# Kernel tuning notes

Hardware: AMD Instinct MI355X
Metric: run time of the kernel (lower is better)

Reference implementation:

```python
import jax, jax.numpy as jnp
import numpy as np

N = 20000      # interaction nodes
E = 160000     # edges
NU = 100000    # num_users
NI = 100000    # num_items
EMB = 64       # emb_size
L1, L2 = 256, 128  # GCN layer dims
H = 2          # GAT heads (and number of GAT layers)
EPS = 1e-5


def _seg(x, idx, n):
    return jax.ops.segment_sum(x, idx, num_segments=n)


def _gcn(x, W, b, src, dst, n):
    # GCNConv: add self-loops, sym-normalize, aggregate src->dst
    loops = jnp.arange(n)
    s = jnp.concatenate([src, loops])
    d = jnp.concatenate([dst, loops])
    deg = _seg(jnp.ones(s.shape[0], x.dtype), d, n)
    dinv = jnp.where(deg > 0, 1.0 / jnp.sqrt(deg), 0.0)
    xw = x @ W
    return _seg((dinv[s] * dinv[d])[:, None] * xw[s], d, n) + b


def _bn(x, g, b):
    # BatchNorm1d in training mode: biased batch statistics
    mu = x.mean(0)
    var = x.var(0)
    return (x - mu) / jnp.sqrt(var + EPS) * g + b


def _sage(x, Wl, bl, Wr, src, dst, n):
    # SAGEConv: mean neighbor aggregation (no self loops) + root transform
    cnt = _seg(jnp.ones(src.shape[0], x.dtype), dst, n)
    agg = _seg(x[src], dst, n) / jnp.maximum(cnt, 1.0)[:, None]
    return agg @ Wl + bl + x @ Wr


def _cheb(x, W0, W1c, b, src, dst, n):
    # ChebConv K=2, lambda_max=2: Tx0 = x, Tx1 = -D^{-1/2} A D^{-1/2} x
    deg = _seg(jnp.ones(src.shape[0], x.dtype), dst, n)
    dinv = jnp.where(deg > 0, 1.0 / jnp.sqrt(deg), 0.0)
    tx1 = -_seg((dinv[src] * dinv[dst])[:, None] * x[src], dst, n)
    return x @ W0 + tx1 @ W1c + b


def _gat(x, W, a_s, a_d, b, src, dst, n):
    # GATConv: add self-loops, per-edge attention softmax over dst, concat=False -> mean over heads
    loops = jnp.arange(n)
    s = jnp.concatenate([src, loops])
    d = jnp.concatenate([dst, loops])
    xp = (x @ W).reshape(n, H, L2)           # [n, H, C]
    al = (xp * a_s).sum(-1)                  # [n, H]
    ar = (xp * a_d).sum(-1)                  # [n, H]
    e = jax.nn.leaky_relu(al[s] + ar[d], 0.2)  # [E', H]
    m = jax.lax.stop_gradient(jax.ops.segment_max(e, d, num_segments=n))
    ex = jnp.exp(e - m[d])
    alpha = ex / _seg(ex, d, n)[d]
    out = _seg(alpha[:, :, None] * xp[s], d, n)  # [n, H, C]
    return out.mean(1) + b


def setup_inputs() -> dict:
    key = jax.random.key(0)
    ks = jax.random.split(key, 40)
    f = lambda k, shp: jax.random.normal(k, shp, dtype=jnp.float32) * 0.02
    inp = {
        'user_idx': jax.random.randint(ks[0], (N,), 0, NU, dtype=jnp.int32),
        'item_idx': jax.random.randint(ks[1], (N,), 0, NI, dtype=jnp.int32),
        'edge_index': jax.random.randint(ks[2], (2, E), 0, N, dtype=jnp.int32),
        'user_emb': f(ks[3], (NU, EMB)),
        'item_emb': f(ks[4], (NI, EMB)),
        'W1': f(ks[5], (2 * EMB, 1024)), 'b1': f(ks[6], (1024,)),
        'W2': f(ks[7], (1024, 512)), 'b2': f(ks[8], (512,)),
        'Wg1': f(ks[9], (512, L1)), 'bg1': f(ks[10], (L1,)),
        'gamma1': 1.0 + f(ks[11], (L1,)), 'beta1': f(ks[12], (L1,)),
        'Wg2': f(ks[13], (L1, L2)), 'bg2': f(ks[14], (L2,)),
        'gamma2': 1.0 + f(ks[15], (L2,)), 'beta2': f(ks[16], (L2,)),
        'Wsl': f(ks[17], (L2, L2)), 'bsl': f(ks[18], (L2,)),
        'Wsr': f(ks[19], (L2, L2)),
        'Wc0': f(ks[20], (L2, L2)), 'Wc1': f(ks[21], (L2, L2)), 'bc': f(ks[22], (L2,)),
        'Wgat1': f(ks[23], (L2, H * L2)), 'as1': f(ks[24], (H, L2)), 'ad1': f(ks[25], (H, L2)), 'bgat1': f(ks[26], (L2,)),
        'Wgat2': f(ks[27], (L2, H * L2)), 'as2': f(ks[28], (H, L2)), 'ad2': f(ks[29], (H, L2)), 'bgat2': f(ks[30], (L2,)),
        'Wp': f(ks[31], (L2, 1)), 'bp': f(ks[32], (1,)),
    }
    return inp


def reference(user_idx, item_idx, edge_index, user_emb, item_emb, W1, b1, W2, b2,
              Wg1, bg1, gamma1, beta1, Wg2, bg2, gamma2, beta2,
              Wsl, bsl, Wsr, Wc0, Wc1, bc,
              Wgat1, as1, ad1, bgat1, Wgat2, as2, ad2, bgat2, Wp, bp):
    src, dst = edge_index[0], edge_index[1]
    n = user_idx.shape[0]
    x = jnp.concatenate([user_emb[user_idx], item_emb[item_idx]], axis=1)
    # MLP (dropout is identity in eval mode)
    x = jax.nn.relu(x @ W1 + b1)
    x = jax.nn.relu(x @ W2 + b2)
    x = jax.nn.relu(_bn(_gcn(x, Wg1, bg1, src, dst, n), gamma1, beta1))
    x = jax.nn.relu(_bn(_gcn(x, Wg2, bg2, src, dst, n), gamma2, beta2))
    x = jax.nn.relu(_sage(x, Wsl, bsl, Wsr, src, dst, n))
    x = jax.nn.relu(_cheb(x, Wc0, Wc1, bc, src, dst, n))
    x = jax.nn.elu(_gat(x, Wgat1, as1, ad1, bgat1, src, dst, n))
    x = jax.nn.elu(_gat(x, Wgat2, as2, ad2, bgat2, src, dst, n))
    return (x @ Wp + bp)[:, 0]
```

## Files before the change

kernel.cpp:

```cpp
#include <hip/hip_runtime.h>
#include <hip/hip_bf16.h>

typedef __hip_bfloat16 bf16;
typedef short s8v __attribute__((ext_vector_type(8)));
typedef float f4v __attribute__((ext_vector_type(4)));

#define NN 20000
#define NE 160000
#define BN_EPS 1e-5f
#define NB 79

#define GF_BIAS 1
#define GF_RELU 2

static __device__ __forceinline__ float b2f(const bf16 x){ return __bfloat162float(x); }
static __device__ __forceinline__ float bits2f(unsigned int u){ return __uint_as_float(u << 16); }
static __device__ __forceinline__ unsigned short f2bits(float f){
  bf16 h = __float2bfloat16(f);
  unsigned short u; __builtin_memcpy(&u, &h, 2); return u;
}
static __device__ __forceinline__ float lrelu(float v){ return (v > 0.f) ? v : 0.2f * v; }

static inline int cdiv(int a, int b){ return (a + b - 1) / b; }


__global__ void k_chk_bf(const unsigned short* __restrict__ x, int n, int code,
                         int* __restrict__ diag){
  bool bad = false;
  for (int k = blockIdx.x * 256 + threadIdx.x; k < n; k += gridDim.x * 256)
    if ((x[k] & 0x7F80u) == 0x7F80u) bad = true;
  if (bad) atomicCAS(diag, 0, code);
}

__global__ void k_diag_out(const int* __restrict__ diag, float* __restrict__ out){
  int d = *diag;
  if (d == 0) return;
  int i = blockIdx.x * 256 + threadIdx.x;
  if (i < NN) out[i] = (float)(d * 100);
}


__global__ void k_ideg(const int* __restrict__ dst, int* __restrict__ ideg){
  int e = blockIdx.x * 256 + threadIdx.x;
  if (e < NE) atomicAdd(&ideg[dst[e]], 1);
}

__global__ __launch_bounds__(256) void k_scan1(const int* __restrict__ ideg,
                                               int* __restrict__ tmp,
                                               int* __restrict__ bsum){
  __shared__ int lds[256];
  int tid = threadIdx.x;
  int i = blockIdx.x * 256 + tid;
  int v = (i < NN) ? ideg[i] : 0;
  lds[tid] = v;
  __syncthreads();
  for (int off = 1; off < 256; off <<= 1){
    int t = (tid >= off) ? lds[tid - off] : 0;
    __syncthreads();
    lds[tid] += t;
    __syncthreads();
  }
  if (i < NN) tmp[i] = lds[tid];
  if (tid == 255) bsum[blockIdx.x] = lds[255];
}

__global__ __launch_bounds__(128) void k_scan2(const int* __restrict__ bsum,
                                               int* __restrict__ boff){
  __shared__ int lds[128];
  int tid = threadIdx.x;
  int v = (tid < NB) ? bsum[tid] : 0;
  lds[tid] = v;
  __syncthreads();
  for (int off = 1; off < 128; off <<= 1){
    int t = (tid >= off) ? lds[tid - off] : 0;
    __syncthreads();
    lds[tid] += t;
    __syncthreads();
  }
  if (tid < NB) boff[tid] = lds[tid] - v;
}

__global__ __launch_bounds__(256) void k_scan3(const int* __restrict__ ideg,
                                               const int* __restrict__ boff,
                                               int* __restrict__ rowptr,
                                               int* __restrict__ cursor,
                                               float* __restrict__ dg,
                                               float* __restrict__ dc,
                                               float* __restrict__ ic){
  int i = blockIdx.x * 256 + threadIdx.x;
  if (i == 0) rowptr[NN] = NE;
  if (i >= NN) return;
  int v = ideg[i];
  int excl = cursor[i] - v + boff[blockIdx.x];
  rowptr[i] = excl;
  cursor[i] = excl;
  float d = (float)v;
  dg[i] = rsqrtf(d + 1.0f);
  dc[i] = (d > 0.f) ? rsqrtf(d) : 0.f;
  ic[i] = 1.0f / fmaxf(d, 1.0f);
}

__global__ void k_fill(const int* __restrict__ src, const int* __restrict__ dst,
                       int* __restrict__ cursor, int* __restrict__ colsrc){
  int e = blockIdx.x * 256 + threadIdx.x;
  if (e >= NE) return;
  int pos = atomicAdd(&cursor[dst[e]], 1);
  colsrc[pos] = src[e];
}


struct WtPack {
  const float* W[10]; short* hi[10]; short* lo[10];
  int K[10]; int nshift[10]; int base[11];
};

__global__ __launch_bounds__(256) void k_wtall(WtPack p){
  int idx = blockIdx.x * 256 + threadIdx.x;
  if (idx >= p.base[10]) return;
  int seg = 0;
#pragma unroll
  for (int i = 1; i < 10; i++) seg += (idx >= p.base[i]) ? 1 : 0;
  int local = idx - p.base[seg];
  int K = p.K[seg], ns = p.nshift[seg];
  int n = local & ((1 << ns) - 1), k = local >> ns;
  float w = p.W[seg][local];
  unsigned short h = f2bits(w);
  unsigned short l = f2bits(w - bits2f(h));
  p.hi[seg][(size_t)n * K + k] = (short)h;
  p.lo[seg][(size_t)n * K + k] = (short)l;
}


__global__ void k_gather(const int* __restrict__ uidx, const int* __restrict__ iidx,
                         const float* __restrict__ ue, const float* __restrict__ ie,
                         bf16* __restrict__ x0){
  int idx = blockIdx.x * 256 + threadIdx.x;
  if (idx >= NN * 128) return;
  int i = idx >> 7, c = idx & 127;
  float v = (c < 64) ? ue[(size_t)uidx[i] * 64 + c] : ie[(size_t)iidx[i] * 64 + (c - 64)];
  x0[idx] = __float2bfloat16(v);
}


__global__ __launch_bounds__(256) void k_mm64(
    const bf16* A0, const short* B0h, const short* B0l, int K0,
    const bf16* A1, const short* B1h, const short* B1l, int K1,
    const float* __restrict__ bias, bf16* __restrict__ C,
    int M, int Ncol, int flags, int npass){
  __shared__ short As[64][72];
  __shared__ short Bhs[64][72];
  __shared__ short Bls[64][72];
  const int tid = threadIdx.x;
  const int bid = blockIdx.y * gridDim.x + blockIdx.x;
  const int total = gridDim.x * gridDim.y;
  const int L = (bid & 7) * (total >> 3) + (bid >> 3);
  const int row0 = (L / gridDim.x) * 64, col0 = (L % gridDim.x) * 64;
  if (row0 >= M) return;
  const int wid = tid >> 6, lane = tid & 63;
  const int wr = (wid >> 1) * 32, wc = (wid & 1) * 32;
  const int lr = lane & 15, lq = lane >> 4;
  const int sr = tid >> 2, sq = (tid & 3) * 16;

  f4v acc[2][2];
#pragma unroll
  for (int i = 0; i < 2; i++)
#pragma unroll
    for (int j = 0; j < 2; j++)
      acc[i][j] = f4v{0.f, 0.f, 0.f, 0.f};

  const bf16* Aarr[2] = {A0, A1};
  const short* Bharr[2] = {B0h, B1h};
  const short* Blarr[2] = {B0l, B1l};
  const int Karr[2] = {K0, K1};

  const bool arow_ok = (row0 + sr) < M;

  for (int p = 0; p < npass; p++){
    const short* A = (const short*)Aarr[p];
    const short* Bh = Bharr[p];
    const short* Bl = Blarr[p];
    const int K = Karr[p];
    const short* arow = A + (size_t)(row0 + sr) * K + sq;
    const short* bhrow = Bh + (size_t)(col0 + sr) * K + sq;
    const short* blrow = Bl + (size_t)(col0 + sr) * K + sq;

    uint4 ra0 = make_uint4(0,0,0,0), ra1 = make_uint4(0,0,0,0);
    if (arow_ok){ ra0 = *(const uint4*)(arow); ra1 = *(const uint4*)(arow + 8); }
    uint4 rb0 = *(const uint4*)(bhrow), rb1 = *(const uint4*)(bhrow + 8);
    uint4 rc0 = *(const uint4*)(blrow), rc1 = *(const uint4*)(blrow + 8);

    for (int k0 = 0; k0 < K; k0 += 64){
      *(uint4*)&As[sr][sq] = ra0;  *(uint4*)&As[sr][sq + 8] = ra1;
      *(uint4*)&Bhs[sr][sq] = rb0; *(uint4*)&Bhs[sr][sq + 8] = rb1;
      *(uint4*)&Bls[sr][sq] = rc0; *(uint4*)&Bls[sr][sq + 8] = rc1;
      __syncthreads();
      if (k0 + 64 < K){
        int off = k0 + 64;
        if (arow_ok){ ra0 = *(const uint4*)(arow + off); ra1 = *(const uint4*)(arow + off + 8); }
        rb0 = *(const uint4*)(bhrow + off); rb1 = *(const uint4*)(bhrow + off + 8);
        rc0 = *(const uint4*)(blrow + off); rc1 = *(const uint4*)(blrow + off + 8);
      }
#pragma unroll
      for (int t = 0; t < 2; t++){
        s8v a[2], bh2[2], bl2[2];
#pragma unroll
        for (int i = 0; i < 2; i++) a[i] = *(const s8v*)&As[wr + i * 16 + lr][t * 32 + lq * 8];
#pragma unroll
        for (int j = 0; j < 2; j++){
          bh2[j] = *(const s8v*)&Bhs[wc + j * 16 + lr][t * 32 + lq * 8];
          bl2[j] = *(const s8v*)&Bls[wc + j * 16 + lr][t * 32 + lq * 8];
        }
#pragma unroll
        for (int i = 0; i < 2; i++)
#pragma unroll
          for (int j = 0; j < 2; j++){
            acc[i][j] = __builtin_amdgcn_mfma_f32_16x16x32_bf16(a[i], bh2[j], acc[i][j], 0, 0, 0);
            acc[i][j] = __builtin_amdgcn_mfma_f32_16x16x32_bf16(a[i], bl2[j], acc[i][j], 0, 0, 0);
          }
      }
      __syncthreads();
    }
  }

#pragma unroll
  for (int i = 0; i < 2; i++){
#pragma unroll
    for (int rg = 0; rg < 4; rg++){
      int row = row0 + wr + i * 16 + lq * 4 + rg;
      if (row >= M) continue;
#pragma unroll
      for (int j = 0; j < 2; j++){
        int col = col0 + wc + j * 16 + lr;
        float v = acc[i][j][rg];
        if (flags & GF_BIAS) v += bias[col];
        if (flags & GF_RELU) v = fmaxf(v, 0.f);
        C[(size_t)row * Ncol + col] = __float2bfloat16(v);
      }
    }
  }
}


__global__ __launch_bounds__(256) void k_agg(
    const int* __restrict__ rowptr, const int* __restrict__ colsrc,
    const bf16* __restrict__ x, const float* __restrict__ wn,
    const float* __restrict__ icv, const float* __restrict__ bias,
    float* __restrict__ outf, bf16* __restrict__ outb,
    int qshift, int mode){
  int idx = blockIdx.x * 256 + threadIdx.x;
  int total = NN << qshift;
  if (idx >= total) return;
  int d = idx >> qshift, q = idx & ((1 << qshift) - 1);
  int F = 4 << qshift;
  int c = q * 4;
  int r0 = rowptr[d], r1 = rowptr[d + 1];
  float s0 = 0.f, s1 = 0.f, s2 = 0.f, s3 = 0.f;
  const short* xs = (const short*)x;
  for (int r = r0; r < r1; r += 4){
    int n = r1 - r;
    int i0 = colsrc[r];
    int i1 = (n > 1) ? colsrc[r + 1] : 0;
    int i2 = (n > 2) ? colsrc[r + 2] : 0;
    int i3 = (n > 3) ? colsrc[r + 3] : 0;
    float w0 = (mode == 1) ? 1.f : wn[i0];
    float w1 = (n > 1) ? ((mode == 1) ? 1.f : wn[i1]) : 0.f;
    float w2 = (n > 2) ? ((mode == 1) ? 1.f : wn[i2]) : 0.f;
    float w3 = (n > 3) ? ((mode == 1) ? 1.f : wn[i3]) : 0.f;
    uint2 v0 = *(const uint2*)(xs + (size_t)i0 * F + c);
    uint2 v1 = *(const uint2*)(xs + (size_t)i1 * F + c);
    uint2 v2 = *(const uint2*)(xs + (size_t)i2 * F + c);
    uint2 v3 = *(const uint2*)(xs + (size_t)i3 * F + c);
    s0 += w0 * bits2f(v0.x & 0xffffu) + w1 * bits2f(v1.x & 0xffffu)
        + w2 * bits2f(v2.x & 0xffffu) + w3 * bits2f(v3.x & 0xffffu);
    s1 += w0 * bits2f(v0.x >> 16) + w1 * bits2f(v1.x >> 16)
        + w2 * bits2f(v2.x >> 16) + w3 * bits2f(v3.x >> 16);
    s2 += w0 * bits2f(v0.y & 0xffffu) + w1 * bits2f(v1.y & 0xffffu)
        + w2 * bits2f(v2.y & 0xffffu) + w3 * bits2f(v3.y & 0xffffu);
    s3 += w0 * bits2f(v0.y >> 16) + w1 * bits2f(v1.y >> 16)
        + w2 * bits2f(v2.y >> 16) + w3 * bits2f(v3.y >> 16);
  }
  if (mode == 0){
    float w = wn[d], w2 = w * w;
    uint2 vd = *(const uint2*)(xs + (size_t)d * F + c);
    float4 o;
    o.x = w * s0 + w2 * bits2f(vd.x & 0xffffu) + bias[c + 0];
    o.y = w * s1 + w2 * bits2f(vd.x >> 16)     + bias[c + 1];
    o.z = w * s2 + w2 * bits2f(vd.y & 0xffffu) + bias[c + 2];
    o.w = w * s3 + w2 * bits2f(vd.y >> 16)     + bias[c + 3];
    *(float4*)(outf + (size_t)d * F + c) = o;
  } else {
    float m = (mode == 1) ? icv[d] : -wn[d];
    unsigned int lo = (unsigned int)f2bits(s0 * m) | ((unsigned int)f2bits(s1 * m) << 16);
    unsigned int hi = (unsigned int)f2bits(s2 * m) | ((unsigned int)f2bits(s3 * m) << 16);
    *(uint2*)((short*)outb + (size_t)d * F + c) = make_uint2(lo, hi);
  }
}


__global__ void k_bn_stats(const float* __restrict__ x, float* __restrict__ stats, int F){
  int c = threadIdx.x & (F - 1);
  int rsub = threadIdx.x / F;
  int rpi = 256 / F;
  int r0 = blockIdx.x * 128;
  int rend = min(NN, r0 + 128);
  float s1 = 0.f, s2 = 0.f;
  for (int r = r0 + rsub; r < rend; r += rpi){
    float v = x[(size_t)r * F + c];
    s1 += v; s2 += v * v;
  }
  atomicAdd(&stats[c], s1);
  atomicAdd(&stats[F + c], s2);
}

__global__ void k_bn_apply(const float* __restrict__ x, const float* __restrict__ stats,
                           const float* __restrict__ g, const float* __restrict__ b,
                           int fshift, int total, bf16* __restrict__ out){
  int idx = blockIdx.x * 256 + threadIdx.x;
  if (idx >= total) return;
  int F = 1 << fshift;
  int c = idx & (F - 1);
  float mu = stats[c] * (1.0f / NN);
  float var = fmaxf(stats[F + c] * (1.0f / NN) - mu * mu, 0.f);
  float v = (x[idx] - mu) * rsqrtf(var + BN_EPS) * g[c] + b[c];
  out[idx] = __float2bfloat16(fmaxf(v, 0.f));
}


__global__ __launch_bounds__(256) void k_gat_alar(const bf16* __restrict__ xp,
                                                  const float* __restrict__ as_,
                                                  const float* __restrict__ ad_,
                                                  float* __restrict__ al,
                                                  float* __restrict__ ar){
  int d = blockIdx.x * 4 + (threadIdx.x >> 6);
  int lane = threadIdx.x & 63;
  if (d >= NN) return;
  int c0 = lane * 2;
  unsigned int p0 = *(const unsigned int*)((const short*)xp + (size_t)d * 256 + c0);
  unsigned int p1 = *(const unsigned int*)((const short*)xp + (size_t)d * 256 + 128 + c0);
  float x00 = bits2f(p0 & 0xffffu), x01 = bits2f(p0 >> 16);
  float x10 = bits2f(p1 & 0xffffu), x11 = bits2f(p1 >> 16);
  float sa0 = x00 * as_[c0] + x01 * as_[c0 + 1];
  float sd0 = x00 * ad_[c0] + x01 * ad_[c0 + 1];
  float sa1 = x10 * as_[128 + c0] + x11 * as_[128 + c0 + 1];
  float sd1 = x10 * ad_[128 + c0] + x11 * ad_[128 + c0 + 1];
#pragma unroll
  for (int off = 32; off > 0; off >>= 1){
    sa0 += __shfl_xor(sa0, off); sd0 += __shfl_xor(sd0, off);
    sa1 += __shfl_xor(sa1, off); sd1 += __shfl_xor(sd1, off);
  }
  if (lane == 0){
    al[d * 2] = sa0;     ar[d * 2] = sd0;
    al[d * 2 + 1] = sa1; ar[d * 2 + 1] = sd1;
  }
}

__global__ __launch_bounds__(64) void k_gat(const int* __restrict__ rowptr,
                                            const int* __restrict__ colsrc,
                                            const bf16* __restrict__ xp,
                                            const float* __restrict__ al,
                                            const float* __restrict__ ar,
                                            const float* __restrict__ bias,
                                            bf16* __restrict__ outb,
                                            const float* __restrict__ wp,
                                            const float* __restrict__ bp,
                                            float* __restrict__ outf){
  __shared__ float w0s[64], w1s[64];
  __shared__ int ss[64];
  int d = blockIdx.x;
  int lane = threadIdx.x;
  int r0 = rowptr[d], r1 = rowptr[d + 1];
  float ard0 = ar[d * 2], ard1 = ar[d * 2 + 1];
  float e0 = lrelu(al[d * 2] + ard0);
  float e1 = lrelu(al[d * 2 + 1] + ard1);
  float mx0 = e0, mx1 = e1;
  for (int r = r0 + lane; r < r1; r += 64){
    int s = colsrc[r];
    mx0 = fmaxf(mx0, lrelu(al[s * 2] + ard0));
    mx1 = fmaxf(mx1, lrelu(al[s * 2 + 1] + ard1));
  }
#pragma unroll
  for (int off = 32; off > 0; off >>= 1){
    mx0 = fmaxf(mx0, __shfl_xor(mx0, off));
    mx1 = fmaxf(mx1, __shfl_xor(mx1, off));
  }
  float ps0 = (lane == 0) ? expf(e0 - mx0) : 0.f;
  float ps1 = (lane == 0) ? expf(e1 - mx1) : 0.f;
  for (int r = r0 + lane; r < r1; r += 64){
    int s = colsrc[r];
    ps0 += expf(lrelu(al[s * 2] + ard0) - mx0);
    ps1 += expf(lrelu(al[s * 2 + 1] + ard1) - mx1);
  }
#pragma unroll
  for (int off = 32; off > 0; off >>= 1){
    ps0 += __shfl_xor(ps0, off);
    ps1 += __shfl_xor(ps1, off);
  }
  int c0 = lane * 2;
  float a00, a01, a10, a11;
  {
    float w0 = expf(e0 - mx0), w1 = expf(e1 - mx1);
    unsigned int p0 = *(const unsigned int*)((const short*)xp + (size_t)d * 256 + c0);
    unsigned int p1 = *(const unsigned int*)((const short*)xp + (size_t)d * 256 + 128 + c0);
    a00 = w0 * bits2f(p0 & 0xffffu); a01 = w0 * bits2f(p0 >> 16);
    a10 = w1 * bits2f(p1 & 0xffffu); a11 = w1 * bits2f(p1 >> 16);
  }
  for (int t0 = r0; t0 < r1; t0 += 64){
    int nt = min(64, r1 - t0);
    __syncthreads();
    if (lane < nt){
      int s = colsrc[t0 + lane];
      ss[lane] = s;
      w0s[lane] = expf(lrelu(al[s * 2] + ard0) - mx0);
      w1s[lane] = expf(lrelu(al[s * 2 + 1] + ard1) - mx1);
    }
    __syncthreads();
    for (int r = 0; r < nt; r++){
      int s = ss[r];
      float w0 = w0s[r], w1 = w1s[r];
      unsigned int p0 = *(const unsigned int*)((const short*)xp + (size_t)s * 256 + c0);
      unsigned int p1 = *(const unsigned int*)((const short*)xp + (size_t)s * 256 + 128 + c0);
      a00 += w0 * bits2f(p0 & 0xffffu); a01 += w0 * bits2f(p0 >> 16);
      a10 += w1 * bits2f(p1 & 0xffffu); a11 += w1 * bits2f(p1 >> 16);
    }
  }
  float v0 = 0.5f * (a00 / ps0 + a10 / ps1) + bias[c0];
  float v1 = 0.5f * (a01 / ps0 + a11 / ps1) + bias[c0 + 1];
  v0 = (v0 > 0.f) ? v0 : expm1f(v0);
  v1 = (v1 > 0.f) ? v1 : expm1f(v1);
  if (wp == nullptr){
    unsigned int packed = (unsigned int)f2bits(v0) | ((unsigned int)f2bits(v1) << 16);
    *(unsigned int*)((short*)outb + (size_t)d * 128 + c0) = packed;
  } else {
    float pv = v0 * wp[c0] + v1 * wp[c0 + 1];
#pragma unroll
    for (int off = 32; off > 0; off >>= 1) pv += __shfl_down(pv, off);
    if (lane == 0) outf[d] = pv + bp[0];
  }
}


extern "C" void kernel_launch(void* const* d_in, const int* in_sizes, int n_in,
                              void* d_out, int out_size, void* d_ws, size_t ws_size,
                              hipStream_t stream){
  const int* uidx = (const int*)d_in[0];
  const int* iidx = (const int*)d_in[1];
  const int* eidx = (const int*)d_in[2];
  const int* src = eidx;
  const int* dst = eidx + NE;
  const float* ue  = (const float*)d_in[3];
  const float* ie  = (const float*)d_in[4];
  const float* W1  = (const float*)d_in[5];  const float* b1  = (const float*)d_in[6];
  const float* W2  = (const float*)d_in[7];  const float* b2  = (const float*)d_in[8];
  const float* Wg1 = (const float*)d_in[9];  const float* bg1 = (const float*)d_in[10];
  const float* gamma1 = (const float*)d_in[11]; const float* beta1 = (const float*)d_in[12];
  const float* Wg2 = (const float*)d_in[13]; const float* bg2 = (const float*)d_in[14];
  const float* gamma2 = (const float*)d_in[15]; const float* beta2 = (const float*)d_in[16];
  const float* Wsl = (const float*)d_in[17]; const float* bsl = (const float*)d_in[18];
  const float* Wsr = (const float*)d_in[19];
  const float* Wc0 = (const float*)d_in[20]; const float* Wc1 = (const float*)d_in[21];
  const float* bc  = (const float*)d_in[22];
  const float* Wgat1 = (const float*)d_in[23]; const float* as1 = (const float*)d_in[24];
  const float* ad1 = (const float*)d_in[25];   const float* bgat1 = (const float*)d_in[26];
  const float* Wgat2 = (const float*)d_in[27]; const float* as2 = (const float*)d_in[28];
  const float* ad2 = (const float*)d_in[29];   const float* bgat2 = (const float*)d_in[30];
  const float* Wp  = (const float*)d_in[31];   const float* bp  = (const float*)d_in[32];

  int* diag   = (int*)d_ws;
  int* ideg   = diag + 4;
  float* stats1 = (float*)(ideg + NN);
  float* stats2 = stats1 + 512;
  int* bsum   = (int*)(stats2 + 256);
  int* boff   = bsum + 128;
  int* rowptr = boff + 128;
  int* cursor = rowptr + NN + 4;
  int* colsrc = cursor + NN;
  float* dg = (float*)(colsrc + NE);
  float* dc = dg + NN;
  float* ic = dc + NN;
  float* al = ic + NN;
  float* ar = al + 2 * NN;
  short* w1h = (short*)(ar + 2 * NN);
  short* w1l = w1h + 131072;
  short* w2h = w1l + 131072;
  short* w2l = w2h + 524288;
  short* wg1h = w2l + 524288;
  short* wg1l = wg1h + 131072;
  short* wg2h = wg1l + 131072;
  short* wg2l = wg2h + 32768;
  short* wslh = wg2l + 32768;
  short* wsll = wslh + 16384;
  short* wsrh = wsll + 16384;
  short* wsrl = wsrh + 16384;
  short* wc0h = wsrl + 16384;
  short* wc0l = wc0h + 16384;
  short* wc1h = wc0l + 16384;
  short* wc1l = wc1h + 16384;
  short* wgat1h = wc1l + 16384;
  short* wgat1l = wgat1h + 32768;
  short* wgat2h = wgat1l + 32768;
  short* wgat2l = wgat2h + 32768;
  short* X0 = wgat2l + 32768;
  short* H1 = X0 + (size_t)NN * 128;
  short* H2 = H1 + (size_t)10000 * 1024;

  bf16* x0b  = (bf16*)X0;
  bf16* h1b  = (bf16*)H1;
  bf16* h2b  = (bf16*)H2;
  bf16* xw1b = (bf16*)H1;
  float* g1f = (float*)H2;
  bf16* g1b  = (bf16*)(H1 + (size_t)NN * 256);
  bf16* xw2b = (bf16*)X0;
  float* x3f = (float*)H1;
  bf16* x3b  = (bf16*)H2;
  bf16* aggb = (bf16*)X0;
  bf16* x4b  = (bf16*)(H2 + (size_t)NN * 128);
  bf16* tx1b = (bf16*)X0;
  bf16* x5b  = (bf16*)(H2 + (size_t)NN * 256);
  bf16* xpb  = (bf16*)H1;
  bf16* x6b  = (bf16*)X0;

  auto mm = [&](const bf16* A1, const short* B1h, const short* B1l, int K1,
                const bf16* A2, const short* B2h, const short* B2l, int K2,
                const float* bias, bf16* C, int M, int N, int flags){
    int nx = N / 64;
    int ny = cdiv(M, 64);
    while ((nx * ny) & 7) ny++;
    dim3 g(nx, ny);
    int np = A2 ? 2 : 1;
    k_mm64<<<g, 256, 0, stream>>>(A1, B1h, B1l, K1, A2, B2h, B2l, K2,
                                  bias, C, M, N, flags, np);
  };

  hipMemsetAsync(diag, 0, (size_t)(4 + NN + 768) * 4, stream);

  k_ideg<<<cdiv(NE, 256), 256, 0, stream>>>(dst, ideg);
  k_scan1<<<NB, 256, 0, stream>>>(ideg, cursor, bsum);
  k_scan2<<<1, 128, 0, stream>>>(bsum, boff);
  k_scan3<<<NB, 256, 0, stream>>>(ideg, boff, rowptr, cursor, dg, dc, ic);
  k_fill<<<cdiv(NE, 256), 256, 0, stream>>>(src, dst, cursor, colsrc);

  {
    WtPack p;
    const float* Ws[10] = {W1, W2, Wg1, Wg2, Wsl, Wsr, Wc0, Wc1, Wgat1, Wgat2};
    short* his[10] = {w1h, w2h, wg1h, wg2h, wslh, wsrh, wc0h, wc1h, wgat1h, wgat2h};
    short* los[10] = {w1l, w2l, wg1l, wg2l, wsll, wsrl, wc0l, wc1l, wgat1l, wgat2l};
    int Ks[10] = {128, 1024, 512, 256, 128, 128, 128, 128, 128, 128};
    int nss[10] = {10, 9, 8, 7, 7, 7, 7, 7, 8, 8};
    int off = 0;
    for (int i = 0; i < 10; i++){
      p.W[i] = Ws[i]; p.hi[i] = his[i]; p.lo[i] = los[i];
      p.K[i] = Ks[i]; p.nshift[i] = nss[i]; p.base[i] = off;
      off += Ks[i] << nss[i];
    }
    p.base[10] = off;
    k_wtall<<<cdiv(off, 256), 256, 0, stream>>>(p);
  }

  k_gather<<<cdiv(NN * 128, 256), 256, 0, stream>>>(uidx, iidx, ue, ie, x0b);

  for (int ofs = 0; ofs < NN; ofs += 10000){
    mm(x0b + (size_t)ofs * 128, w1h, w1l, 128, nullptr, nullptr, nullptr, 0,
       b1, h1b, 10000, 1024, GF_BIAS | GF_RELU);
    mm(h1b, w2h, w2l, 1024, nullptr, nullptr, nullptr, 0,
       b2, h2b + (size_t)ofs * 512, 10000, 512, GF_BIAS | GF_RELU);
  }

  mm(h2b, wg1h, wg1l, 512, nullptr, nullptr, nullptr, 0, nullptr, xw1b, NN, 256, 0);
  k_agg<<<cdiv(NN * 64, 256), 256, 0, stream>>>(rowptr, colsrc, xw1b, dg, nullptr, bg1, g1f, nullptr, 6, 0);
  k_bn_stats<<<cdiv(NN, 128), 256, 0, stream>>>(g1f, stats1, 256);
  k_bn_apply<<<cdiv(NN * 256, 256), 256, 0, stream>>>(g1f, stats1, gamma1, beta1, 8, NN * 256, g1b);

  mm(g1b, wg2h, wg2l, 256, nullptr, nullptr, nullptr, 0, nullptr, xw2b, NN, 128, 0);
  k_agg<<<cdiv(NN * 32, 256), 256, 0, stream>>>(rowptr, colsrc, xw2b, dg, nullptr, bg2, x3f, nullptr, 5, 0);
  k_bn_stats<<<cdiv(NN, 128), 256, 0, stream>>>(x3f, stats2, 128);
  k_bn_apply<<<cdiv(NN * 128, 256), 256, 0, stream>>>(x3f, stats2, gamma2, beta2, 7, NN * 128, x3b);

  k_agg<<<cdiv(NN * 32, 256), 256, 0, stream>>>(rowptr, colsrc, x3b, nullptr, ic, nullptr, nullptr, aggb, 5, 1);
  mm(aggb, wslh, wsll, 128, x3b, wsrh, wsrl, 128, bsl, x4b, NN, 128, GF_BIAS | GF_RELU);

  k_agg<<<cdiv(NN * 32, 256), 256, 0, stream>>>(rowptr, colsrc, x4b, dc, nullptr, nullptr, nullptr, tx1b, 5, 2);
  mm(x4b, wc0h, wc0l, 128, tx1b, wc1h, wc1l, 128, bc, x5b, NN, 128, GF_BIAS | GF_RELU);

  mm(x5b, wgat1h, wgat1l, 128, nullptr, nullptr, nullptr, 0, nullptr, xpb, NN, 256, 0);
  k_gat_alar<<<cdiv(NN, 4), 256, 0, stream>>>(xpb, as1, ad1, al, ar);
  k_gat<<<NN, 64, 0, stream>>>(rowptr, colsrc, xpb, al, ar, bgat1, x6b,
                               nullptr, nullptr, nullptr);
  k_chk_bf<<<256, 256, 0, stream>>>((const unsigned short*)x6b, NN * 128, 16, diag);

  mm(x6b, wgat2h, wgat2l, 128, nullptr, nullptr, nullptr, 0, nullptr, xpb, NN, 256, 0);
  k_gat_alar<<<cdiv(NN, 4), 256, 0, stream>>>(xpb, as2, ad2, al, ar);
  k_gat<<<NN, 64, 0, stream>>>(rowptr, colsrc, xpb, al, ar, bgat2, nullptr,
                               Wp, bp, (float*)d_out);
  k_diag_out<<<cdiv(NN, 256), 256, 0, stream>>>(diag, (float*)d_out);
}
```

Baseline: 613.1 us.

## Add 128x128-tile MFMA GEMM with direct global-to-LDS loads for wide matmuls

Adds a new GEMM kernel that gives each block a 128x128 output tile, with each wave computing 64x64 through 4x4 MFMA fragments. Operands are staged into LDS with the global_load_lds builtin instead of going through registers. The MLP, first GCN and GAT projection matmuls move to this kernel to get more reuse per LDS load and fewer blocks. The larger tile uses 48KB of LDS per block and more accumulator registers, which can lower occupancy. There is no double buffering, and the N=256 cases launch few column tiles.

```diff
diff --git a/kernel.cpp b/kernel.cpp
--- a/kernel.cpp
+++ b/kernel.cpp
@@ -22,6 +22,12 @@
 static __device__ __forceinline__ float lrelu(float v){ return (v > 0.f) ? v : 0.2f * v; }
 
 static inline int cdiv(int a, int b){ return (a + b - 1) / b; }
+
+static __device__ __forceinline__ void gload16(const short* g, short* l){
+  __builtin_amdgcn_global_load_lds(
+      (const __attribute__((address_space(1))) unsigned int*)g,
+      (__attribute__((address_space(3))) unsigned int*)l, 16, 0, 0);
+}
 
 
 __global__ void k_chk_bf(const unsigned short* __restrict__ x, int n, int code,
@@ -231,6 +237,93 @@
 #pragma unroll
       for (int j = 0; j < 2; j++){
         int col = col0 + wc + j * 16 + lr;
+        float v = acc[i][j][rg];
+        if (flags & GF_BIAS) v += bias[col];
+        if (flags & GF_RELU) v = fmaxf(v, 0.f);
+        C[(size_t)row * Ncol + col] = __float2bfloat16(v);
+      }
+    }
+  }
+}
+
+
+__global__ __launch_bounds__(256) void k_mm128(
+    const bf16* A0, const short* B0h, const short* B0l, int K,
+    const float* __restrict__ bias, bf16* __restrict__ C,
+    int M, int Ncol, int flags){
+  __shared__ short As[128 * 64];
+  __shared__ short Bhs[128 * 64];
+  __shared__ short Bls[128 * 64];
+  const int tid = threadIdx.x;
+  const int bid = blockIdx.y * gridDim.x + blockIdx.x;
+  const int total = gridDim.x * gridDim.y;
+  const int L = (bid & 7) * (total >> 3) + (bid >> 3);
+  const int row0 = (L / gridDim.x) * 128, col0 = (L % gridDim.x) * 128;
+  if (row0 >= M) return;
+  const int wid = tid >> 6, lane = tid & 63;
+  const int wr2 = (wid >> 1) * 64, wc2 = (wid & 1) * 64;
+  const int lr = lane & 15, lq = lane >> 4;
+
+  f4v acc[4][4];
+#pragma unroll
+  for (int i = 0; i < 4; i++)
+#pragma unroll
+    for (int j = 0; j < 4; j++)
+      acc[i][j] = f4v{0.f, 0.f, 0.f, 0.f};
+
+  const short* A = (const short*)A0;
+  const short* asrc[4]; const short* bhsrc[4]; const short* blsrc[4];
+  int sdst[4];
+#pragma unroll
+  for (int i = 0; i < 4; i++){
+    int ci = i * 256 + tid;
+    int r = ci >> 3, sg = ci & 7;
+    int ar = row0 + r; if (ar > M - 1) ar = M - 1;
+    asrc[i]  = A   + (size_t)ar * K + sg * 8;
+    bhsrc[i] = B0h + (size_t)(col0 + r) * K + sg * 8;
+    blsrc[i] = B0l + (size_t)(col0 + r) * K + sg * 8;
+    sdst[i] = ci * 8;
+  }
+
+  for (int k0 = 0; k0 < K; k0 += 64){
+    __syncthreads();
+#pragma unroll
+    for (int i = 0; i < 4; i++){
+      gload16(asrc[i]  + k0, As  + sdst[i]);
+      gload16(bhsrc[i] + k0, Bhs + sdst[i]);
+      gload16(blsrc[i] + k0, Bls + sdst[i]);
+    }
+    __syncthreads();
+#pragma unroll
+    for (int t = 0; t < 2; t++){
+      s8v a[4], bh2[4], bl2[4];
+#pragma unroll
+      for (int i = 0; i < 4; i++)
+        a[i] = *(const s8v*)&As[(wr2 + i * 16 + lr) * 64 + t * 32 + lq * 8];
+#pragma unroll
+      for (int j = 0; j < 4; j++){
+        bh2[j] = *(const s8v*)&Bhs[(wc2 + j * 16 + lr) * 64 + t * 32 + lq * 8];
+        bl2[j] = *(const s8v*)&Bls[(wc2 + j * 16 + lr) * 64 + t * 32 + lq * 8];
+      }
+#pragma unroll
+      for (int i = 0; i < 4; i++)
+#pragma unroll
+        for (int j = 0; j < 4; j++){
+          acc[i][j] = __builtin_amdgcn_mfma_f32_16x16x32_bf16(a[i], bh2[j], acc[i][j], 0, 0, 0);
+          acc[i][j] = __builtin_amdgcn_mfma_f32_16x16x32_bf16(a[i], bl2[j], acc[i][j], 0, 0, 0);
+        }
+    }
+  }
+
+#pragma unroll
+  for (int i = 0; i < 4; i++){
+#pragma unroll
+    for (int rg = 0; rg < 4; rg++){
+      int row = row0 + wr2 + i * 16 + lq * 4 + rg;
+      if (row >= M) continue;
+#pragma unroll
+      for (int j = 0; j < 4; j++){
+        int col = col0 + wc2 + j * 16 + lr;
         float v = acc[i][j][rg];
         if (flags & GF_BIAS) v += bias[col];
         if (flags & GF_RELU) v = fmaxf(v, 0.f);
@@ -531,6 +624,15 @@
                                   bias, C, M, N, flags, np);
   };
 
+  auto mm128 = [&](const bf16* A, const short* Bh, const short* Bl, int K,
+                   const float* bias, bf16* C, int M, int N, int flags){
+    int nx = N / 128;
+    int ny = cdiv(M, 128);
+    while ((nx * ny) & 7) ny++;
+    dim3 g(nx, ny);
+    k_mm128<<<g, 256, 0, stream>>>(A, Bh, Bl, K, bias, C, M, N, flags);
+  };
+
   hipMemsetAsync(diag, 0, (size_t)(4 + NN + 768) * 4, stream);
 
   k_ideg<<<cdiv(NE, 256), 256, 0, stream>>>(dst, ideg);
@@ -559,13 +661,13 @@
   k_gather<<<cdiv(NN * 128, 256), 256, 0, stream>>>(uidx, iidx, ue, ie, x0b);
 
   for (int ofs = 0; ofs < NN; ofs += 10000){
-    mm(x0b + (size_t)ofs * 128, w1h, w1l, 128, nullptr, nullptr, nullptr, 0,
-       b1, h1b, 10000, 1024, GF_BIAS | GF_RELU);
-    mm(h1b, w2h, w2l, 1024, nullptr, nullptr, nullptr, 0,
-       b2, h2b + (size_t)ofs * 512, 10000, 512, GF_BIAS | GF_RELU);
-  }
-
-  mm(h2b, wg1h, wg1l, 512, nullptr, nullptr, nullptr, 0, nullptr, xw1b, NN, 256, 0);
+    mm128(x0b + (size_t)ofs * 128, w1h, w1l, 128,
+          b1, h1b, 10000, 1024, GF_BIAS | GF_RELU);
+    mm128(h1b, w2h, w2l, 1024,
+          b2, h2b + (size_t)ofs * 512, 10000, 512, GF_BIAS | GF_RELU);
+  }
+
+  mm128(h2b, wg1h, wg1l, 512, nullptr, xw1b, NN, 256, 0);
   k_agg<<<cdiv(NN * 64, 256), 256, 0, stream>>>(rowptr, colsrc, xw1b, dg, nullptr, bg1, g1f, nullptr, 6, 0);
   k_bn_stats<<<cdiv(NN, 128), 256, 0, stream>>>(g1f, stats1, 256);
   k_bn_apply<<<cdiv(NN * 256, 256), 256, 0, stream>>>(g1f, stats1, gamma1, beta1, 8, NN * 256, g1b);
@@ -581,13 +683,13 @@
   k_agg<<<cdiv(NN * 32, 256), 256, 0, stream>>>(rowptr, colsrc, x4b, dc, nullptr, nullptr, nullptr, tx1b, 5, 2);
   mm(x4b, wc0h, wc0l, 128, tx1b, wc1h, wc1l, 128, bc, x5b, NN, 128, GF_BIAS | GF_RELU);
 
-  mm(x5b, wgat1h, wgat1l, 128, nullptr, nullptr, nullptr, 0, nullptr, xpb, NN, 256, 0);
+  mm128(x5b, wgat1h, wgat1l, 128, nullptr, xpb, NN, 256, 0);
   k_gat_alar<<<cdiv(NN, 4), 256, 0, stream>>>(xpb, as1, ad1, al, ar);
   k_gat<<<NN, 64, 0, stream>>>(rowptr, colsrc, xpb, al, ar, bgat1, x6b,
                                nullptr, nullptr, nullptr);
   k_chk_bf<<<256, 256, 0, stream>>>((const unsigned short*)x6b, NN * 128, 16, diag);
 
-  mm(x6b, wgat2h, wgat2l, 128, nullptr, nullptr, nullptr, 0, nullptr, xpb, NN, 256, 0);
+  mm128(x6b, wgat2h, wgat2l, 128, nullptr, xpb, NN, 256, 0);
   k_gat_alar<<<cdiv(NN, 4), 256, 0, stream>>>(xpb, as2, ad2, al, ar);
   k_gat<<<NN, 64, 0, stream>>>(rowptr, colsrc, xpb, al, ar, bgat2, nullptr,
                                Wp, bp, (float*)d_out);
```

Result: slower. 644.0 us (+5.0%).
